# Kernel optimization log

Measured on AMD Instinct MI355X. Metric: run time of the kernel, lower is better.

The kernel has to match this reference:

```python
import jax, jax.numpy as jnp
import numpy as np

N_NODES = 50000
HIDDEN = 64
N_EDGES = 1200000


def setup_inputs() -> dict:
    key = jax.random.key(0)
    ks = jax.random.split(key, 12)
    x = jax.random.normal(ks[0], (N_NODES, HIDDEN), dtype=jnp.float32)
    edge_index = jax.random.randint(ks[1], (2, N_EDGES), 0, N_NODES, dtype=jnp.int64)
    s = 1.0 / np.sqrt(HIDDEN)
    # RGCN layer (single relation): relation weight, root weight, bias
    W_rel1 = jax.random.normal(ks[2], (HIDDEN, HIDDEN), dtype=jnp.float32) * s
    W_root1 = jax.random.normal(ks[3], (HIDDEN, HIDDEN), dtype=jnp.float32) * s
    b1 = jnp.zeros((HIDDEN,), dtype=jnp.float32)
    # Three GraphConv layers: self weight, neighbor weight, bias each
    W_self2 = jax.random.normal(ks[4], (HIDDEN, HIDDEN), dtype=jnp.float32) * s
    W_nbr2 = jax.random.normal(ks[5], (HIDDEN, HIDDEN), dtype=jnp.float32) * s
    b2 = jnp.zeros((HIDDEN,), dtype=jnp.float32)
    W_self3 = jax.random.normal(ks[6], (HIDDEN, HIDDEN), dtype=jnp.float32) * s
    W_nbr3 = jax.random.normal(ks[7], (HIDDEN, HIDDEN), dtype=jnp.float32) * s
    b3 = jnp.zeros((HIDDEN,), dtype=jnp.float32)
    W_self4 = jax.random.normal(ks[8], (HIDDEN, HIDDEN), dtype=jnp.float32) * s
    W_nbr4 = jax.random.normal(ks[9], (HIDDEN, HIDDEN), dtype=jnp.float32) * s
    b4 = jnp.zeros((HIDDEN,), dtype=jnp.float32)
    return {
        "x": x, "edge_index": edge_index,
        "W_rel1": W_rel1, "W_root1": W_root1, "b1": b1,
        "W_self2": W_self2, "W_nbr2": W_nbr2, "b2": b2,
        "W_self3": W_self3, "W_nbr3": W_nbr3, "b3": b3,
        "W_self4": W_self4, "W_nbr4": W_nbr4, "b4": b4,
    }


def _rgcn(x, W_rel, W_root, b, src, dst, n_nodes):
    # single-relation RGCN: root transform + mean-aggregated relation transform
    msg = x[src] @ W_rel                                   # [E, H]
    agg = jax.ops.segment_sum(msg, dst, num_segments=n_nodes)
    cnt = jax.ops.segment_sum(jnp.ones((src.shape[0],), x.dtype), dst, num_segments=n_nodes)
    agg = agg / jnp.maximum(cnt, 1.0)[:, None]
    return x @ W_root + agg + b


def _graphconv(x, W_self, W_nbr, b, src, dst, n_nodes):
    # GraphConv: self transform + sum-aggregated neighbor transform
    agg = jax.ops.segment_sum(x[src], dst, num_segments=n_nodes)  # [N, H]
    return x @ W_self + agg @ W_nbr + b


def reference(x, edge_index, W_rel1, W_root1, b1, W_self2, W_nbr2, b2,
              W_self3, W_nbr3, b3, W_self4, W_nbr4, b4):
    n = x.shape[0]
    src, dst = edge_index[0], edge_index[1]
    h = jax.nn.relu(_rgcn(x, W_rel1, W_root1, b1, src, dst, n))
    h = jax.nn.relu(_graphconv(h, W_self2, W_nbr2, b2, src, dst, n))
    x_1 = h
    h = jax.nn.relu(_graphconv(h, W_self3, W_nbr3, b3, src, dst, n))
    h = jax.nn.relu(_graphconv(h, W_self4, W_nbr4, b4, src, dst, n))
    x_2 = h
    return (x_1, x_2)
```

## Files before the change

kernel.cpp:

```cpp
#include <hip/hip_runtime.h>

#define N_NODES 50000
#define HIDDEN  64
#define N_EDGES 1200000

#define BSHIFT 7
#define BUKSZ  128
#define NBUK   391
#define GBIN   256
#define PAD2   4096
#define FWAVES 12500
#define FBLK   (FWAVES / 4)
#define NPW    4

typedef unsigned short ushort_t;

__device__ __forceinline__ float bcastf(float v, int k) {
    return __int_as_float(__builtin_amdgcn_readlane(__float_as_int(v), k));
}
__device__ __forceinline__ unsigned f2bf(float x) {
    unsigned u = __float_as_uint(x);
    u += 0x7fffu + ((u >> 16) & 1u);
    return u >> 16;
}
__device__ __forceinline__ float bfl(unsigned w) { return __uint_as_float(w << 16); }
__device__ __forceinline__ float bfh(unsigned w) { return __uint_as_float(w & 0xffff0000u); }
__device__ __forceinline__ void bfly(float4& a) {
    a.x += __shfl_xor(a.x, 16); a.y += __shfl_xor(a.y, 16);
    a.z += __shfl_xor(a.z, 16); a.w += __shfl_xor(a.w, 16);
    a.x += __shfl_xor(a.x, 32); a.y += __shfl_xor(a.y, 32);
    a.z += __shfl_xor(a.z, 32); a.w += __shfl_xor(a.w, 32);
}

__global__ __launch_bounds__(512) void init_kernel(int* __restrict__ cursor,
                                                   const float* __restrict__ Wn2, const float* __restrict__ Ws2,
                                                   const float* __restrict__ Wn3, const float* __restrict__ Ws3,
                                                   const float* __restrict__ Wn4, const float* __restrict__ Ws4,
                                                   uint4* __restrict__ pw) {
    int b = blockIdx.x, tid = threadIdx.x;
    if (b == 0) {
        if (tid < NBUK) cursor[tid] = tid * PAD2;
    } else {
        int layer = b - 1;
        const float* Wn = (layer == 0) ? Wn2 : (layer == 1) ? Wn3 : Wn4;
        const float* Ws = (layer == 0) ? Ws2 : (layer == 1) ? Ws3 : Ws4;
        for (int e = tid; e < 1024; e += 512) {
            const float4 a = *(const float4*)(Wn + e * 4);
            const float4 c = *(const float4*)(Ws + e * 4);
            uint4 o;
            o.x = f2bf(a.x) | (f2bf(a.y) << 16);
            o.y = f2bf(a.z) | (f2bf(a.w) << 16);
            o.z = f2bf(c.x) | (f2bf(c.y) << 16);
            o.w = f2bf(c.z) | (f2bf(c.w) << 16);
            pw[layer * 1024 + e] = o;
        }
    }
}

__global__ __launch_bounds__(256) void scatter_fused_kernel(const int* __restrict__ ei,
                                                            int* __restrict__ cursor,
                                                            int* __restrict__ tmp, int E) {
    __shared__ int h[NBUK];
    __shared__ int cur[NBUK];
    int tid = threadIdx.x;
    for (int b = tid; b < NBUK; b += 256) h[b] = 0;
    __syncthreads();
    for (int e = blockIdx.x * 256 + tid; e < E; e += GBIN * 256)
        atomicAdd(&h[ei[E + e] >> BSHIFT], 1);
    __syncthreads();
    for (int b = tid; b < NBUK; b += 256) cur[b] = atomicAdd(&cursor[b], h[b]);
    __syncthreads();
    for (int e = blockIdx.x * 256 + tid; e < E; e += GBIN * 256) {
        int src = ei[e];
        int dst = ei[E + e];
        int p = atomicAdd(&cur[dst >> BSHIFT], 1);
        tmp[p] = src | ((dst & (BUKSZ - 1)) << 16);
    }
}

__global__ __launch_bounds__(512) void bucketize_kernel(const int* __restrict__ tmp,
                                                        const int* __restrict__ cursor,
                                                        int2* __restrict__ row_info,
                                                        ushort_t* __restrict__ csr,
                                                        const float* __restrict__ x,
                                                        const float* __restrict__ Wrel,
                                                        const float* __restrict__ Wroot,
                                                        const float* __restrict__ bias,
                                                        ushort_t* __restrict__ tbf,
                                                        ushort_t* __restrict__ ubf) {
    __shared__ int hist[BUKSZ];
    __shared__ int cur[BUKSZ];
    __shared__ ushort_t stage[PAD2];
    int b = blockIdx.x, tid = threadIdx.x;
    if (b < NBUK) {
        int base = b * PAD2;
        int count = cursor[b] - base;
        int node_base = b << BSHIFT;
        if (tid < BUKSZ) hist[tid] = 0;
        __syncthreads();
        for (int i = tid; i < count; i += 512)
            atomicAdd(&hist[tmp[base + i] >> 16], 1);
        __syncthreads();
        int v = (tid < BUKSZ) ? hist[tid] : 0;
        int vr = (v + 3) & ~3;
        __syncthreads();
        if (tid < BUKSZ) hist[tid] = vr;
#pragma unroll
        for (int o = 1; o < BUKSZ; o <<= 1) {
            __syncthreads();
            int y = (tid >= o && tid < BUKSZ) ? hist[tid - o] : 0;
            __syncthreads();
            if (tid < BUKSZ) hist[tid] += y;
        }
        __syncthreads();
        if (tid < BUKSZ) {
            int excl = hist[tid] - vr;
            cur[tid] = excl;
            int node = node_base + tid;
            if (node < N_NODES) row_info[node] = make_int2(base + excl, v);
        }
        __syncthreads();
        for (int i = tid; i < count; i += 512) {
            int p = tmp[base + i];
            int slot = atomicAdd(&cur[p >> 16], 1);
            stage[slot] = (ushort_t)(p & 0xFFFF);
        }
        __syncthreads();
        int total = hist[BUKSZ - 1];
        for (int i = tid; i < total; i += 512)
            csr[base + i] = stage[i];
    } else {
        int lane = tid & 63;
        float wn[64], ws[64];
#pragma unroll
        for (int k = 0; k < 64; ++k) {
            wn[k] = Wrel[k * 64 + lane];
            ws[k] = Wroot[k * 64 + lane];
        }
        float bv = bias[lane];
        int wave = (b - NBUK) * 8 + (tid >> 6);
        int nwaves = (gridDim.x - NBUK) * 8;
        if (wave == 0) tbf[(size_t)N_NODES * 64 + lane] = 0;
        for (int i = wave; i < N_NODES; i += nwaves) {
            float hv = x[i * 64 + lane];
            float tacc = 0.f, uacc = bv;
#pragma unroll
            for (int k = 0; k < 64; ++k) {
                float hk = bcastf(hv, k);
                tacc = fmaf(hk, wn[k], tacc);
                uacc = fmaf(hk, ws[k], uacc);
            }
            tbf[(size_t)i * 64 + lane] = (ushort_t)f2bf(tacc);
            ubf[(size_t)i * 64 + lane] = (ushort_t)f2bf(uacc);
        }
    }
}

__device__ __forceinline__ float4 agg_core(const ushort_t* __restrict__ tbf,
                                           const ushort_t* __restrict__ csr,
                                           int start, int deg, int g, int q) {
    const ushort_t* cp = csr + start;
    float4 a0{0,0,0,0}, a1{0,0,0,0}, a2{0,0,0,0}, a3{0,0,0,0};
    for (int base = 0; base < deg; base += 16) {
        int m = base + 4 * g;
        const uint2 iv = *(const uint2*)(cp + m);
        int s0 = (m + 0 < deg) ? (int)(iv.x & 0xFFFF) : N_NODES;
        int s1 = (m + 1 < deg) ? (int)(iv.x >> 16)    : N_NODES;
        int s2 = (m + 2 < deg) ? (int)(iv.y & 0xFFFF) : N_NODES;
        int s3 = (m + 3 < deg) ? (int)(iv.y >> 16)    : N_NODES;
        const uint2 w0 = *(const uint2*)(tbf + (size_t)s0 * 64 + q * 4);
        const uint2 w1 = *(const uint2*)(tbf + (size_t)s1 * 64 + q * 4);
        const uint2 w2 = *(const uint2*)(tbf + (size_t)s2 * 64 + q * 4);
        const uint2 w3 = *(const uint2*)(tbf + (size_t)s3 * 64 + q * 4);
        a0.x += bfl(w0.x); a0.y += bfh(w0.x); a0.z += bfl(w0.y); a0.w += bfh(w0.y);
        a1.x += bfl(w1.x); a1.y += bfh(w1.x); a1.z += bfl(w1.y); a1.w += bfh(w1.y);
        a2.x += bfl(w2.x); a2.y += bfh(w2.x); a2.z += bfl(w2.y); a2.w += bfh(w2.y);
        a3.x += bfl(w3.x); a3.y += bfh(w3.x); a3.z += bfl(w3.y); a3.w += bfh(w3.y);
    }
    float4 acc;
    acc.x = (a0.x + a1.x) + (a2.x + a3.x);
    acc.y = (a0.y + a1.y) + (a2.y + a3.y);
    acc.z = (a0.z + a1.z) + (a2.z + a3.z);
    acc.w = (a0.w + a1.w) + (a2.w + a3.w);
    bfly(acc);
    return acc;
}

__device__ __forceinline__ float4 unpack_u(const ushort_t* __restrict__ ubf, int node, int q) {
    const uint2 uv = *(const uint2*)(ubf + (size_t)node * 64 + q * 4);
    return make_float4(bfl(uv.x), bfh(uv.x), bfl(uv.y), bfh(uv.y));
}

__global__ __launch_bounds__(256, 6) void fused_kernel(const ushort_t* __restrict__ tin,
                                                       const ushort_t* __restrict__ uin,
                                                       const int2* __restrict__ row_info,
                                                       const ushort_t* __restrict__ csr,
                                                       const uint4* __restrict__ pwL,
                                                       const float* __restrict__ bias_next,
                                                       ushort_t* __restrict__ tout,
                                                       ushort_t* __restrict__ uout,
                                                       float* __restrict__ dout,
                                                       int use_mean) {
    __shared__ uint4 wlds[1024];
    __shared__ float blds[64];
    int tid = threadIdx.x;
    for (int i = tid; i < 1024; i += 256) wlds[i] = pwL[i];
    if (tid < 64) blds[tid] = bias_next[tid];
    if (blockIdx.x == 0 && tid < 32)
        ((unsigned*)(tout + (size_t)N_NODES * 64))[tid] = 0;
    __syncthreads();
    int lane = tid & 63, g = lane >> 4, q = lane & 15;
    int w = blockIdx.x * 4 + (tid >> 6);

#pragma unroll
    for (int i = 0; i < NPW; ++i) {
        int node = w + FWAVES * i;
        if (node >= N_NODES) continue;
        int2 ri = row_info[node];
        float4 acc = agg_core(tin, csr, ri.x, ri.y, g, q);
        float sc = use_mean ? 1.f / fmaxf((float)ri.y, 1.f) : 1.f;
        const float4 uv = unpack_u(uin, node, q);
        float4 h;
        h.x = fmaxf(uv.x + acc.x * sc, 0.f);
        h.y = fmaxf(uv.y + acc.y * sc, 0.f);
        h.z = fmaxf(uv.z + acc.z * sc, 0.f);
        h.w = fmaxf(uv.w + acc.w * sc, 0.f);
        if (dout && g == 0)
            *(float4*)(dout + (size_t)node * 64 + q * 4) = h;
        float4 tp{0,0,0,0}, up{0,0,0,0};
#pragma unroll
        for (int j = 0; j < 16; ++j) {
            uint4 wv = wlds[(16 * g + j) * 16 + q];
            int srcl = 4 * g + (j >> 2);
            float hk;
            if ((j & 3) == 0)      hk = __shfl(h.x, srcl);
            else if ((j & 3) == 1) hk = __shfl(h.y, srcl);
            else if ((j & 3) == 2) hk = __shfl(h.z, srcl);
            else                   hk = __shfl(h.w, srcl);
            tp.x = fmaf(hk, bfl(wv.x), tp.x); tp.y = fmaf(hk, bfh(wv.x), tp.y);
            tp.z = fmaf(hk, bfl(wv.y), tp.z); tp.w = fmaf(hk, bfh(wv.y), tp.w);
            up.x = fmaf(hk, bfl(wv.z), up.x); up.y = fmaf(hk, bfh(wv.z), up.y);
            up.z = fmaf(hk, bfl(wv.w), up.z); up.w = fmaf(hk, bfh(wv.w), up.w);
        }
        bfly(tp); bfly(up);
        if (g == 0) {
            const float4 bv = *(const float4*)&blds[q * 4];
            uint2 upk, tpk;
            upk.x = f2bf(up.x + bv.x) | (f2bf(up.y + bv.y) << 16);
            upk.y = f2bf(up.z + bv.z) | (f2bf(up.w + bv.w) << 16);
            tpk.x = f2bf(tp.x) | (f2bf(tp.y) << 16);
            tpk.y = f2bf(tp.z) | (f2bf(tp.w) << 16);
            *(uint2*)(uout + (size_t)node * 64 + q * 4) = upk;
            *(uint2*)(tout + (size_t)node * 64 + q * 4) = tpk;
        }
    }
}

__global__ __launch_bounds__(256, 8) void agg_kernel(const ushort_t* __restrict__ tbf,
                                                     const ushort_t* __restrict__ ubf,
                                                     const int2* __restrict__ row_info,
                                                     const ushort_t* __restrict__ csr,
                                                     float* __restrict__ out, int use_mean) {
    int lane = threadIdx.x & 63;
    int g = lane >> 4, q = lane & 15;
    int node = (blockIdx.x * 256 + threadIdx.x) >> 6;
    if (node >= N_NODES) return;
    int2 ri = row_info[node];
    float4 acc = agg_core(tbf, csr, ri.x, ri.y, g, q);
    float scale = use_mean ? 1.f / fmaxf((float)ri.y, 1.f) : 1.f;
    if (g == 0) {
        const float4 uv = unpack_u(ubf, node, q);
        float4 r;
        r.x = fmaxf(uv.x + acc.x * scale, 0.f);
        r.y = fmaxf(uv.y + acc.y * scale, 0.f);
        r.z = fmaxf(uv.z + acc.z * scale, 0.f);
        r.w = fmaxf(uv.w + acc.w * scale, 0.f);
        *(float4*)(out + (size_t)node * 64 + q * 4) = r;
    }
}

extern "C" void kernel_launch(void* const* d_in, const int* in_sizes, int n_in,
                              void* d_out, int out_size, void* d_ws, size_t ws_size,
                              hipStream_t stream) {
    const float* x      = (const float*)d_in[0];
    const int*   ei     = (const int*)d_in[1];
    const float* Wrel1  = (const float*)d_in[2];
    const float* Wroot1 = (const float*)d_in[3];
    const float* b1     = (const float*)d_in[4];
    const float* Wself2 = (const float*)d_in[5];
    const float* Wnbr2  = (const float*)d_in[6];
    const float* b2     = (const float*)d_in[7];
    const float* Wself3 = (const float*)d_in[8];
    const float* Wnbr3  = (const float*)d_in[9];
    const float* b3     = (const float*)d_in[10];
    const float* Wself4 = (const float*)d_in[11];
    const float* Wnbr4  = (const float*)d_in[12];
    const float* b4     = (const float*)d_in[13];

    const int N = N_NODES, E = N_EDGES;

    auto align = [](size_t o) { return (o + 255) & ~(size_t)255; };
    char* base = (char*)d_ws;
    size_t off = 0;
    int*  cursor   = (int*)(base + off);  off = align(off + (size_t)NBUK * 4);
    int2* row_info = (int2*)(base + off); off = align(off + (size_t)N * 8);
    int*  tmp      = (int*)(base + off);  off = align(off + (size_t)NBUK * PAD2 * 4);
    ushort_t* csr  = (ushort_t*)(base + off); off = align(off + (size_t)NBUK * PAD2 * 2 + 1024);
    uint4* pw      = (uint4*)(base + off);    off = align(off + (size_t)3 * 1024 * 16);
    ushort_t* tbA  = (ushort_t*)(base + off); off = align(off + (size_t)(N + 1) * 64 * 2);
    ushort_t* tbB  = (ushort_t*)(base + off); off = align(off + (size_t)(N + 1) * 64 * 2);
    ushort_t* ubA  = (ushort_t*)(base + off); off = align(off + (size_t)N * 64 * 2);
    ushort_t* ubB  = (ushort_t*)(base + off); off = align(off + (size_t)N * 64 * 2);

    float* out1 = (float*)d_out;
    float* out2 = (float*)d_out + (size_t)N * 64;

    init_kernel<<<4, 512, 0, stream>>>(cursor, Wnbr2, Wself2, Wnbr3, Wself3, Wnbr4, Wself4, pw);
    scatter_fused_kernel<<<GBIN, 256, 0, stream>>>(ei, cursor, tmp, E);
    bucketize_kernel<<<NBUK + 1024, 512, 0, stream>>>(tmp, cursor, row_info, csr,
                                                      x, Wrel1, Wroot1, b1, tbA, ubA);
    fused_kernel<<<FBLK, 256, 0, stream>>>(tbA, ubA, row_info, csr, pw,        b2, tbB, ubB, nullptr, 1);
    fused_kernel<<<FBLK, 256, 0, stream>>>(tbB, ubB, row_info, csr, pw + 1024, b3, tbA, ubA, out1, 0);
    fused_kernel<<<FBLK, 256, 0, stream>>>(tbA, ubA, row_info, csr, pw + 2048, b4, tbB, ubB, nullptr, 0);
    agg_kernel<<<(N + 3) / 4, 256, 0, stream>>>(tbB, ubB, row_info, csr, out2, 0);
}
```

Measured before the change: 336.2 us.

## Switch bf16 intermediates to fp16 with packed-half accumulation and fdot2 transforms

Replaces the bf16 storage of transformed node features with fp16 and accumulates neighbor sums in packed half2 registers instead of fp32. The per-node 64x64 transform now uses fdot2 on half2 pairs with a reorganized weight packing. CSR rows are padded to multiples of 16 with a dummy zero node, so the aggregation loop drops its per-element bounds checks. This cuts ALU and conversion work in the gather loop, at the cost of fp16 range and accumulation-precision risk and a larger padded CSR buffer.

```diff
diff --git a/kernel.cpp b/kernel.cpp
--- a/kernel.cpp
+++ b/kernel.cpp
@@ -1,4 +1,5 @@
 #include <hip/hip_runtime.h>
+#include <hip/hip_fp16.h>
 
 #define N_NODES 50000
 #define HIDDEN  64
@@ -8,23 +9,27 @@
 #define BUKSZ  128
 #define NBUK   391
 #define GBIN   256
-#define PAD2   4096
+#define PAD2   6144
 #define FWAVES 12500
 #define FBLK   (FWAVES / 4)
 #define NPW    4
 
 typedef unsigned short ushort_t;
+typedef _Float16 hf2 __attribute__((ext_vector_type(2)));
 
 __device__ __forceinline__ float bcastf(float v, int k) {
     return __int_as_float(__builtin_amdgcn_readlane(__float_as_int(v), k));
 }
-__device__ __forceinline__ unsigned f2bf(float x) {
-    unsigned u = __float_as_uint(x);
-    u += 0x7fffu + ((u >> 16) & 1u);
-    return u >> 16;
-}
-__device__ __forceinline__ float bfl(unsigned w) { return __uint_as_float(w << 16); }
-__device__ __forceinline__ float bfh(unsigned w) { return __uint_as_float(w & 0xffff0000u); }
+__device__ __forceinline__ hf2 u2h(unsigned u) { union { unsigned u; hf2 h; } x; x.u = u; return x.h; }
+__device__ __forceinline__ unsigned h2u(hf2 h) { union { hf2 h; unsigned u; } x; x.h = h; return x.u; }
+__device__ __forceinline__ unsigned pkh(float a, float b) {
+    __half2 h = __float22half2_rn(make_float2(a, b));
+    union { __half2 h; unsigned u; } x; x.h = h; return x.u;
+}
+__device__ __forceinline__ ushort_t f2h(float a) {
+    __half h = __float2half_rn(a);
+    union { __half h; ushort_t u; } x; x.h = h; return x.u;
+}
 __device__ __forceinline__ void bfly(float4& a) {
     a.x += __shfl_xor(a.x, 16); a.y += __shfl_xor(a.y, 16);
     a.z += __shfl_xor(a.z, 16); a.w += __shfl_xor(a.w, 16);
@@ -44,15 +49,16 @@
         int layer = b - 1;
         const float* Wn = (layer == 0) ? Wn2 : (layer == 1) ? Wn3 : Wn4;
         const float* Ws = (layer == 0) ? Ws2 : (layer == 1) ? Ws3 : Ws4;
-        for (int e = tid; e < 1024; e += 512) {
-            const float4 a = *(const float4*)(Wn + e * 4);
-            const float4 c = *(const float4*)(Ws + e * 4);
-            uint4 o;
-            o.x = f2bf(a.x) | (f2bf(a.y) << 16);
-            o.y = f2bf(a.z) | (f2bf(a.w) << 16);
-            o.z = f2bf(c.x) | (f2bf(c.y) << 16);
-            o.w = f2bf(c.z) | (f2bf(c.w) << 16);
-            pw[layer * 1024 + e] = o;
+        int kp = tid >> 4, q = tid & 15;
+        {
+            const float4 a = *(const float4*)(Wn + (2 * kp) * 64 + 4 * q);
+            const float4 c = *(const float4*)(Wn + (2 * kp + 1) * 64 + 4 * q);
+            pw[layer * 1024 + tid] = make_uint4(pkh(a.x, c.x), pkh(a.y, c.y), pkh(a.z, c.z), pkh(a.w, c.w));
+        }
+        {
+            const float4 a = *(const float4*)(Ws + (2 * kp) * 64 + 4 * q);
+            const float4 c = *(const float4*)(Ws + (2 * kp + 1) * 64 + 4 * q);
+            pw[layer * 1024 + 512 + tid] = make_uint4(pkh(a.x, c.x), pkh(a.y, c.y), pkh(a.z, c.z), pkh(a.w, c.w));
         }
     }
 }
@@ -102,7 +108,7 @@
             atomicAdd(&hist[tmp[base + i] >> 16], 1);
         __syncthreads();
         int v = (tid < BUKSZ) ? hist[tid] : 0;
-        int vr = (v + 3) & ~3;
+        int vr = (v + 15) & ~15;
         __syncthreads();
         if (tid < BUKSZ) hist[tid] = vr;
 #pragma unroll
@@ -113,13 +119,17 @@
             if (tid < BUKSZ) hist[tid] += y;
         }
         __syncthreads();
+        int excl = 0;
         if (tid < BUKSZ) {
-            int excl = hist[tid] - vr;
+            excl = hist[tid] - vr;
             cur[tid] = excl;
             int node = node_base + tid;
             if (node < N_NODES) row_info[node] = make_int2(base + excl, v);
         }
         __syncthreads();
+        if (tid < BUKSZ) {
+            for (int p = v; p < vr; ++p) stage[excl + p] = (ushort_t)N_NODES;
+        }
         for (int i = tid; i < count; i += 512) {
             int p = tmp[base + i];
             int slot = atomicAdd(&cur[p >> 16], 1);
@@ -150,8 +160,8 @@
                 tacc = fmaf(hk, wn[k], tacc);
                 uacc = fmaf(hk, ws[k], uacc);
             }
-            tbf[(size_t)i * 64 + lane] = (ushort_t)f2bf(tacc);
-            ubf[(size_t)i * 64 + lane] = (ushort_t)f2bf(uacc);
+            tbf[(size_t)i * 64 + lane] = f2h(tacc);
+            ubf[(size_t)i * 64 + lane] = f2h(uacc);
         }
     }
 }
@@ -160,35 +170,36 @@
                                            const ushort_t* __restrict__ csr,
                                            int start, int deg, int g, int q) {
     const ushort_t* cp = csr + start;
-    float4 a0{0,0,0,0}, a1{0,0,0,0}, a2{0,0,0,0}, a3{0,0,0,0};
-    for (int base = 0; base < deg; base += 16) {
+    hf2 l0{0,0}, l1{0,0}, l2{0,0}, l3{0,0};
+    hf2 m0{0,0}, m1{0,0}, m2{0,0}, m3{0,0};
+    int vr = (deg + 15) & ~15;
+    for (int base = 0; base < vr; base += 16) {
         int m = base + 4 * g;
         const uint2 iv = *(const uint2*)(cp + m);
-        int s0 = (m + 0 < deg) ? (int)(iv.x & 0xFFFF) : N_NODES;
-        int s1 = (m + 1 < deg) ? (int)(iv.x >> 16)    : N_NODES;
-        int s2 = (m + 2 < deg) ? (int)(iv.y & 0xFFFF) : N_NODES;
-        int s3 = (m + 3 < deg) ? (int)(iv.y >> 16)    : N_NODES;
+        int s0 = (int)(iv.x & 0xFFFF);
+        int s1 = (int)(iv.x >> 16);
+        int s2 = (int)(iv.y & 0xFFFF);
+        int s3 = (int)(iv.y >> 16);
         const uint2 w0 = *(const uint2*)(tbf + (size_t)s0 * 64 + q * 4);
         const uint2 w1 = *(const uint2*)(tbf + (size_t)s1 * 64 + q * 4);
         const uint2 w2 = *(const uint2*)(tbf + (size_t)s2 * 64 + q * 4);
         const uint2 w3 = *(const uint2*)(tbf + (size_t)s3 * 64 + q * 4);
-        a0.x += bfl(w0.x); a0.y += bfh(w0.x); a0.z += bfl(w0.y); a0.w += bfh(w0.y);
-        a1.x += bfl(w1.x); a1.y += bfh(w1.x); a1.z += bfl(w1.y); a1.w += bfh(w1.y);
-        a2.x += bfl(w2.x); a2.y += bfh(w2.x); a2.z += bfl(w2.y); a2.w += bfh(w2.y);
-        a3.x += bfl(w3.x); a3.y += bfh(w3.x); a3.z += bfl(w3.y); a3.w += bfh(w3.y);
-    }
-    float4 acc;
-    acc.x = (a0.x + a1.x) + (a2.x + a3.x);
-    acc.y = (a0.y + a1.y) + (a2.y + a3.y);
-    acc.z = (a0.z + a1.z) + (a2.z + a3.z);
-    acc.w = (a0.w + a1.w) + (a2.w + a3.w);
+        l0 += u2h(w0.x); m0 += u2h(w0.y);
+        l1 += u2h(w1.x); m1 += u2h(w1.y);
+        l2 += u2h(w2.x); m2 += u2h(w2.y);
+        l3 += u2h(w3.x); m3 += u2h(w3.y);
+    }
+    hf2 lo = (l0 + l1) + (l2 + l3);
+    hf2 hi = (m0 + m1) + (m2 + m3);
+    float4 acc = make_float4((float)lo.x, (float)lo.y, (float)hi.x, (float)hi.y);
     bfly(acc);
     return acc;
 }
 
 __device__ __forceinline__ float4 unpack_u(const ushort_t* __restrict__ ubf, int node, int q) {
     const uint2 uv = *(const uint2*)(ubf + (size_t)node * 64 + q * 4);
-    return make_float4(bfl(uv.x), bfh(uv.x), bfl(uv.y), bfh(uv.y));
+    hf2 a = u2h(uv.x), b = u2h(uv.y);
+    return make_float4((float)a.x, (float)a.y, (float)b.x, (float)b.y);
 }
 
 __global__ __launch_bounds__(256, 6) void fused_kernel(const ushort_t* __restrict__ tin,
@@ -227,29 +238,34 @@
         h.w = fmaxf(uv.w + acc.w * sc, 0.f);
         if (dout && g == 0)
             *(float4*)(dout + (size_t)node * 64 + q * 4) = h;
+        int hp_lo = (int)pkh(h.x, h.y);
+        int hp_hi = (int)pkh(h.z, h.w);
         float4 tp{0,0,0,0}, up{0,0,0,0};
 #pragma unroll
-        for (int j = 0; j < 16; ++j) {
-            uint4 wv = wlds[(16 * g + j) * 16 + q];
-            int srcl = 4 * g + (j >> 2);
-            float hk;
-            if ((j & 3) == 0)      hk = __shfl(h.x, srcl);
-            else if ((j & 3) == 1) hk = __shfl(h.y, srcl);
-            else if ((j & 3) == 2) hk = __shfl(h.z, srcl);
-            else                   hk = __shfl(h.w, srcl);
-            tp.x = fmaf(hk, bfl(wv.x), tp.x); tp.y = fmaf(hk, bfh(wv.x), tp.y);
-            tp.z = fmaf(hk, bfl(wv.y), tp.z); tp.w = fmaf(hk, bfh(wv.y), tp.w);
-            up.x = fmaf(hk, bfl(wv.z), up.x); up.y = fmaf(hk, bfh(wv.z), up.y);
-            up.z = fmaf(hk, bfl(wv.w), up.z); up.w = fmaf(hk, bfh(wv.w), up.w);
+        for (int jp = 0; jp < 8; ++jp) {
+            int kp = 8 * g + jp;
+            const uint4 wvn = wlds[kp * 16 + q];
+            const uint4 wvs = wlds[512 + kp * 16 + q];
+            int srcl = 4 * g + (jp >> 1);
+            unsigned hu = (unsigned)__shfl((jp & 1) ? hp_hi : hp_lo, srcl);
+            hf2 hh = u2h(hu);
+            tp.x = __builtin_amdgcn_fdot2(hh, u2h(wvn.x), tp.x, false);
+            tp.y = __builtin_amdgcn_fdot2(hh, u2h(wvn.y), tp.y, false);
+            tp.z = __builtin_amdgcn_fdot2(hh, u2h(wvn.z), tp.z, false);
+            tp.w = __builtin_amdgcn_fdot2(hh, u2h(wvn.w), tp.w, false);
+            up.x = __builtin_amdgcn_fdot2(hh, u2h(wvs.x), up.x, false);
+            up.y = __builtin_amdgcn_fdot2(hh, u2h(wvs.y), up.y, false);
+            up.z = __builtin_amdgcn_fdot2(hh, u2h(wvs.z), up.z, false);
+            up.w = __builtin_amdgcn_fdot2(hh, u2h(wvs.w), up.w, false);
         }
         bfly(tp); bfly(up);
         if (g == 0) {
             const float4 bv = *(const float4*)&blds[q * 4];
             uint2 upk, tpk;
-            upk.x = f2bf(up.x + bv.x) | (f2bf(up.y + bv.y) << 16);
-            upk.y = f2bf(up.z + bv.z) | (f2bf(up.w + bv.w) << 16);
-            tpk.x = f2bf(tp.x) | (f2bf(tp.y) << 16);
-            tpk.y = f2bf(tp.z) | (f2bf(tp.w) << 16);
+            upk.x = pkh(up.x + bv.x, up.y + bv.y);
+            upk.y = pkh(up.z + bv.z, up.w + bv.w);
+            tpk.x = pkh(tp.x, tp.y);
+            tpk.y = pkh(tp.z, tp.w);
             *(uint2*)(uout + (size_t)node * 64 + q * 4) = upk;
             *(uint2*)(tout + (size_t)node * 64 + q * 4) = tpk;
         }
```

Result: faster. 280.2 us (-16.7%).
